# Performance work log

Measured on AMD Instinct MI355X. Metric: run time of the kernel, lower is better.

## Reference

```python
import jax, jax.numpy as jnp
import numpy as np

NUM_FIELDS = 24
OP = "circular_convolution"  # or "circular_correlation"

# upper-triangular (i<j) field pair indices, matching torch.triu_indices(F, F, offset=1)
_I, _J = np.triu_indices(NUM_FIELDS, k=1)
_IDX0 = jnp.asarray(_I, dtype=jnp.int32)  # [P], P = F*(F-1)/2 = 276
_IDX1 = jnp.asarray(_J, dtype=jnp.int32)


def setup_inputs() -> dict:
    key = jax.random.key(0)
    inputs = jax.random.normal(key, (2048, NUM_FIELDS, 64), dtype=jnp.float32)
    return {"inputs": inputs}


def reference(inputs):
    # inputs: [B, F, D]; gather pairwise field embeddings -> [B, P, D]
    emb0 = inputs[:, _IDX0, :]
    emb1 = inputs[:, _IDX1, :]
    fft0 = jnp.fft.fft(emb0)  # complex64, FFT along D
    fft1 = jnp.fft.fft(emb1)
    if OP == "circular_correlation":
        fft0 = jnp.conj(fft0)
    # circular convolution/correlation via frequency-domain product; real part of ifft
    return jnp.real(jnp.fft.ifft(fft0 * fft1))  # [B, P, D]
```

## Files before the change

kernel.cpp:

```cpp
#include <hip/hip_runtime.h>
#include <stdint.h>


typedef __bf16 bf16x8 __attribute__((ext_vector_type(8)));
typedef float  f32x4  __attribute__((ext_vector_type(4)));

#define NF       24
#define DIM      64
#define NPAIR    276
#define RSTRIDE  264
#define XB_OFF   (NF * RSTRIDE)
#define XB_STRIDE 72
#define LDS_BYTES (XB_OFF + 32 * XB_STRIDE * 2)

__global__ __launch_bounds__(256)
void holo_fm_kernel(const float* __restrict__ in, float* __restrict__ out)
{
    __shared__ __align__(16) unsigned char lds[LDS_BYTES];
    __bf16* xb = (__bf16*)(lds + XB_OFF);

    const int tid = threadIdx.x;
    const int b   = blockIdx.x;
    const float* xin = in + (size_t)b * (NF * DIM);

    for (int e = tid; e < (32 - NF) * XB_STRIDE; e += 256)
        xb[NF * XB_STRIDE + e] = (__bf16)0.0f;

    for (int e = tid; e < NF * DIM; e += 256) {
        int f = e >> 6, m = e & 63;
        __bf16 v = (__bf16)xin[e];
        xb[f * XB_STRIDE + m] = v;
        __bf16* rr = (__bf16*)(lds + f * RSTRIDE);
        int u0 = (64 - m) & 63;
        rr[u0]      = v;
        rr[u0 + 64] = v;
    }
    __syncthreads();

    const int lane = tid & 63;
    const int wave = tid >> 6;
    const int ln   = lane & 15;
    const int q    = lane >> 4;

    bf16x8 bfrag[2][2];
    #pragma unroll
    for (int jt = 0; jt < 2; ++jt)
        #pragma unroll
        for (int ks = 0; ks < 2; ++ks)
            bfrag[jt][ks] = *(const bf16x8*)(xb + (jt * 16 + ln) * XB_STRIDE + ks * 32 + q * 8);

    float* gbase = out + (size_t)b * NPAIR * DIM;

    for (int i = wave; i < NF - 1; i += 4) {
        const uint64_t* ri = (const uint64_t*)(lds + i * RSTRIDE);
        const int p0 = 23 * i - (i * (i - 1)) / 2;

        bf16x8 awin[6];
        #pragma unroll
        for (int w = 0; w < 6; ++w) {
            int ob = 2 * (16 * (w + 1) + 8 * q - ln);
            int dw = ob >> 3;
            int sh = (ob & 7) * 8;
            uint64_t w0 = ri[dw], w1 = ri[dw + 1], w2 = ri[dw + 2];
            uint64_t lo = (w0 >> sh) | ((w1 << 1) << (63 - sh));
            uint64_t hi = (w1 >> sh) | ((w2 << 1) << (63 - sh));
            union { uint64_t u[2]; bf16x8 v; } cv;
            cv.u[0] = lo; cv.u[1] = hi;
            awin[w] = cv.v;
        }

        const int jtlo = (i < 15) ? 0 : 1;
        for (int jt = jtlo; jt < 2; ++jt) {
            const int j = 16 * jt + ln;
            const bool valid = (j > i) & (j < NF);
            float* orow = gbase + ((size_t)(p0 + j - i - 1)) * DIM + 4 * q;
            #pragma unroll
            for (int mt = 0; mt < 4; ++mt) {
                f32x4 c = {0.f, 0.f, 0.f, 0.f};
                c = __builtin_amdgcn_mfma_f32_16x16x32_bf16(awin[3 - mt], bfrag[jt][0], c, 0, 0, 0);
                c = __builtin_amdgcn_mfma_f32_16x16x32_bf16(awin[5 - mt], bfrag[jt][1], c, 0, 0, 0);
                if (valid)
                    *(f32x4*)(orow + 16 * mt) = c;
            }
        }
    }
}

extern "C" void kernel_launch(void* const* d_in, const int* in_sizes, int n_in,
                              void* d_out, int out_size, void* d_ws, size_t ws_size,
                              hipStream_t stream)
{
    const float* in  = (const float*)d_in[0];
    float*       out = (float*)d_out;
    const int batches = in_sizes[0] / (NF * DIM);
    holo_fm_kernel<<<dim3(batches), dim3(256), 0, stream>>>(in, out);
}
```

Before: 159.1 us.

## Process four batches per block with double-buffered LDS and register prefetch

Each block now handles four batch rows instead of one. The next batch's inputs are prefetched into registers while the current one is computed, using two LDS buffers. Output stores become nontemporal, and launch bounds request two blocks per SM. The aim is to hide global load latency and amortise per-block setup. The cost is fewer blocks (512) on a large GPU, which may reduce parallelism, plus more LDS per block.

```diff
diff --git a/kernel.cpp b/kernel.cpp
--- a/kernel.cpp
+++ b/kernel.cpp
@@ -5,83 +5,117 @@
 typedef __bf16 bf16x8 __attribute__((ext_vector_type(8)));
 typedef float  f32x4  __attribute__((ext_vector_type(4)));
 
-#define NF       24
-#define DIM      64
-#define NPAIR    276
-#define RSTRIDE  264
-#define XB_OFF   (NF * RSTRIDE)
+#define NF        24
+#define DIM       64
+#define NPAIR     276
+#define RSTRIDE   264
+#define XB_OFF    (NF * RSTRIDE)
 #define XB_STRIDE 72
-#define LDS_BYTES (XB_OFF + 32 * XB_STRIDE * 2)
+#define BUF_BYTES (XB_OFF + 32 * XB_STRIDE * 2)
+#define BPB       4
 
-__global__ __launch_bounds__(256)
-void holo_fm_kernel(const float* __restrict__ in, float* __restrict__ out)
+__global__ __launch_bounds__(256, 2)
+void holo_fm_kernel(const float* __restrict__ in, float* __restrict__ out, int batches)
 {
-    __shared__ __align__(16) unsigned char lds[LDS_BYTES];
-    __bf16* xb = (__bf16*)(lds + XB_OFF);
+    __shared__ __align__(16) unsigned char lds[2 * BUF_BYTES];
 
-    const int tid = threadIdx.x;
-    const int b   = blockIdx.x;
-    const float* xin = in + (size_t)b * (NF * DIM);
-
-    for (int e = tid; e < (32 - NF) * XB_STRIDE; e += 256)
-        xb[NF * XB_STRIDE + e] = (__bf16)0.0f;
-
-    for (int e = tid; e < NF * DIM; e += 256) {
-        int f = e >> 6, m = e & 63;
-        __bf16 v = (__bf16)xin[e];
-        xb[f * XB_STRIDE + m] = v;
-        __bf16* rr = (__bf16*)(lds + f * RSTRIDE);
-        int u0 = (64 - m) & 63;
-        rr[u0]      = v;
-        rr[u0 + 64] = v;
-    }
-    __syncthreads();
-
+    const int tid  = threadIdx.x;
     const int lane = tid & 63;
     const int wave = tid >> 6;
     const int ln   = lane & 15;
     const int q    = lane >> 4;
+    const int b0   = blockIdx.x * BPB;
 
-    bf16x8 bfrag[2][2];
     #pragma unroll
-    for (int jt = 0; jt < 2; ++jt)
+    for (int buf = 0; buf < 2; ++buf) {
+        __bf16* xb = (__bf16*)(lds + buf * BUF_BYTES + XB_OFF);
+        for (int e = tid; e < (32 - NF) * XB_STRIDE; e += 256)
+            xb[NF * XB_STRIDE + e] = (__bf16)0.0f;
+    }
+
+    auto loadRegs = [&](float* dst, int batch) {
+        const float* xin = in + (size_t)batch * (NF * DIM);
         #pragma unroll
-        for (int ks = 0; ks < 2; ++ks)
-            bfrag[jt][ks] = *(const bf16x8*)(xb + (jt * 16 + ln) * XB_STRIDE + ks * 32 + q * 8);
+        for (int r = 0; r < 6; ++r) dst[r] = xin[tid + 256 * r];
+    };
 
-    float* gbase = out + (size_t)b * NPAIR * DIM;
+    auto stage = [&](int buf, const float* vals) {
+        unsigned char* base = lds + buf * BUF_BYTES;
+        __bf16* xb = (__bf16*)(base + XB_OFF);
+        #pragma unroll
+        for (int r = 0; r < 6; ++r) {
+            int e = tid + 256 * r;
+            int f = e >> 6, m = e & 63;
+            __bf16 v = (__bf16)vals[r];
+            xb[f * XB_STRIDE + m] = v;
+            __bf16* rr = (__bf16*)(base + f * RSTRIDE);
+            int u0 = (64 - m) & 63;
+            rr[u0]      = v;
+            rr[u0 + 64] = v;
+        }
+    };
 
-    for (int i = wave; i < NF - 1; i += 4) {
-        const uint64_t* ri = (const uint64_t*)(lds + i * RSTRIDE);
-        const int p0 = 23 * i - (i * (i - 1)) / 2;
+    auto compute = [&](int buf, int batch) {
+        const unsigned char* base = lds + buf * BUF_BYTES;
+        const __bf16* xb = (const __bf16*)(base + XB_OFF);
 
-        bf16x8 awin[6];
+        bf16x8 bfrag[2][2];
         #pragma unroll
-        for (int w = 0; w < 6; ++w) {
-            int ob = 2 * (16 * (w + 1) + 8 * q - ln);
-            int dw = ob >> 3;
-            int sh = (ob & 7) * 8;
-            uint64_t w0 = ri[dw], w1 = ri[dw + 1], w2 = ri[dw + 2];
-            uint64_t lo = (w0 >> sh) | ((w1 << 1) << (63 - sh));
-            uint64_t hi = (w1 >> sh) | ((w2 << 1) << (63 - sh));
-            union { uint64_t u[2]; bf16x8 v; } cv;
-            cv.u[0] = lo; cv.u[1] = hi;
-            awin[w] = cv.v;
+        for (int jt = 0; jt < 2; ++jt)
+            #pragma unroll
+            for (int ks = 0; ks < 2; ++ks)
+                bfrag[jt][ks] = *(const bf16x8*)(xb + (jt * 16 + ln) * XB_STRIDE + ks * 32 + q * 8);
+
+        float* gbase = out + (size_t)batch * NPAIR * DIM;
+
+        for (int i = wave; i < NF - 1; i += 4) {
+            const uint64_t* ri = (const uint64_t*)(base + i * RSTRIDE);
+            const int p0 = 23 * i - (i * (i - 1)) / 2;
+
+            bf16x8 awin[6];
+            #pragma unroll
+            for (int w = 0; w < 6; ++w) {
+                int ob = 2 * (16 * (w + 1) + 8 * q - ln);
+                int dw = ob >> 3;
+                int sh = (ob & 7) * 8;
+                uint64_t w0 = ri[dw], w1 = ri[dw + 1], w2 = ri[dw + 2];
+                uint64_t lo = (w0 >> sh) | ((w1 << 1) << (63 - sh));
+                uint64_t hi = (w1 >> sh) | ((w2 << 1) << (63 - sh));
+                union { uint64_t u[2]; bf16x8 v; } cv;
+                cv.u[0] = lo; cv.u[1] = hi;
+                awin[w] = cv.v;
+            }
+
+            const int jtlo = (i < 15) ? 0 : 1;
+            for (int jt = jtlo; jt < 2; ++jt) {
+                const int j = 16 * jt + ln;
+                const bool valid = (j > i) & (j < NF);
+                float* orow = gbase + ((size_t)(p0 + j - i - 1)) * DIM + 4 * q;
+                #pragma unroll
+                for (int mt = 0; mt < 4; ++mt) {
+                    f32x4 c = {0.f, 0.f, 0.f, 0.f};
+                    c = __builtin_amdgcn_mfma_f32_16x16x32_bf16(awin[3 - mt], bfrag[jt][0], c, 0, 0, 0);
+                    c = __builtin_amdgcn_mfma_f32_16x16x32_bf16(awin[5 - mt], bfrag[jt][1], c, 0, 0, 0);
+                    if (valid)
+                        __builtin_nontemporal_store(c, (f32x4*)(orow + 16 * mt));
+                }
+            }
         }
+    };
 
-        const int jtlo = (i < 15) ? 0 : 1;
-        for (int jt = jtlo; jt < 2; ++jt) {
-            const int j = 16 * jt + ln;
-            const bool valid = (j > i) & (j < NF);
-            float* orow = gbase + ((size_t)(p0 + j - i - 1)) * DIM + 4 * q;
-            #pragma unroll
-            for (int mt = 0; mt < 4; ++mt) {
-                f32x4 c = {0.f, 0.f, 0.f, 0.f};
-                c = __builtin_amdgcn_mfma_f32_16x16x32_bf16(awin[3 - mt], bfrag[jt][0], c, 0, 0, 0);
-                c = __builtin_amdgcn_mfma_f32_16x16x32_bf16(awin[5 - mt], bfrag[jt][1], c, 0, 0, 0);
-                if (valid)
-                    *(f32x4*)(orow + 16 * mt) = c;
-            }
+    float pa[6], pb[6];
+    loadRegs(pa, b0);
+    stage(0, pa);
+    if (b0 + 1 < batches) loadRegs(pb, b0 + 1);
+    __syncthreads();
+
+    #pragma unroll
+    for (int t = 0; t < BPB; ++t) {
+        if (b0 + t < batches) compute(t & 1, b0 + t);
+        if (t + 1 < BPB) {
+            if (b0 + t + 1 < batches) stage((t + 1) & 1, (t & 1) ? pa : pb);
+            if (t + 2 < BPB && b0 + t + 2 < batches) loadRegs((t & 1) ? pb : pa, b0 + t + 2);
+            __syncthreads();
         }
     }
 }
@@ -93,5 +127,6 @@
     const float* in  = (const float*)d_in[0];
     float*       out = (float*)d_out;
     const int batches = in_sizes[0] / (NF * DIM);
-    holo_fm_kernel<<<dim3(batches), dim3(256), 0, stream>>>(in, out);
+    const int blocks  = (batches + BPB - 1) / BPB;
+    holo_fm_kernel<<<dim3(blocks), dim3(256), 0, stream>>>(in, out, batches);
 }
```

New measurement: 234.1 us. 47.1% more time.
